# Kernel optimization log

Hardware: AMD Instinct MI355X
Metric: run time of the kernel (lower is better)

The kernel has to match this reference:

```python
import jax, jax.numpy as jnp
import numpy as np

B, I, H = 512, 256, 512
UNFOLDS = 6


def setup_inputs() -> dict:
    key = jax.random.key(0)
    ks = jax.random.split(key, 13)
    u = lambda k, shape, lo, hi: jax.random.uniform(k, shape, jnp.float32, lo, hi)
    sensory_erev = (2.0 * jax.random.randint(ks[3], (I, H), 0, 2) - 1.0).astype(jnp.float32)
    erev = (2.0 * jax.random.randint(ks[7], (H, H), 0, 2) - 1.0).astype(jnp.float32)
    return {
        "inputs": jax.random.normal(ks[0], (B, I), jnp.float32),
        "state": jax.random.normal(ks[1], (B, H), jnp.float32),
        "sensory_mu": u(ks[2], (I, H), 0.3, 0.8),
        "sensory_sigma": u(ks[4], (I, H), 3.0, 8.0),
        "sensory_W": u(ks[5], (I, H), 0.01, 1.0),
        "sensory_erev": sensory_erev,
        "mu": u(ks[6], (H, H), 0.3, 0.8),
        "sigma": u(ks[8], (H, H), 3.0, 8.0),
        "W": u(ks[9], (H, H), 0.01, 1.0),
        "erev": erev,
        "vleak": u(ks[10], (H,), -0.2, 0.2),
        "gleak": jnp.ones((H,), jnp.float32),
        "cm": jnp.full((H,), 0.5, jnp.float32),
    }


def reference(inputs, state, sensory_mu, sensory_sigma, sensory_W, sensory_erev,
              mu, sigma, W, erev, vleak, gleak, cm):
    # Sensory synapse currents (computed once): (B, I, H) broadcast
    sensory_act = jax.nn.sigmoid((inputs[:, :, None] - sensory_mu[None]) * sensory_sigma[None])
    sensory_w_act = sensory_W[None] * sensory_act                      # (B, I, H)
    w_num_sensory = jnp.sum(sensory_w_act * sensory_erev[None], axis=1)  # (B, H)
    w_den_sensory = jnp.sum(sensory_w_act, axis=1)                        # (B, H)

    def step(v_pre, _):
        # recurrent synapse gating: (B, H_pre, H_post)
        act = jax.nn.sigmoid((v_pre[:, :, None] - mu[None]) * sigma[None])
        w_act = W[None] * act
        w_num = jnp.sum(w_act * erev[None], axis=1) + w_num_sensory
        w_den = jnp.sum(w_act, axis=1) + w_den_sensory
        numerator = cm * v_pre + gleak * vleak + w_num
        denominator = cm + gleak + w_den
        return numerator / (denominator + 1e-8), None

    v_pre, _ = jax.lax.scan(step, state, None, length=UNFOLDS)
    return v_pre
```

## Files before the change

kernel.cpp:

```cpp
#include <hip/hip_runtime.h>

#define LTC_B 512
#define LTC_H 512
#define LTC_I 256

static constexpr float kL2E = 1.4426950408889634f;

struct alignas(16) HPair { _Float16 a0, a1, c0, c1, wz0, wz1, wd0, wd1; };

typedef unsigned int u32;
#define AS_G __attribute__((address_space(1)))
#define AS_L __attribute__((address_space(3)))

__device__ __forceinline__ void ldg_lds16(const void* g, void* l) {
    __builtin_amdgcn_global_load_lds((const AS_G u32*)g, (AS_L u32*)l, 16, 0, 0);
}

template<int K>
__global__ void ltc_prep(const float* __restrict__ mu, const float* __restrict__ sigma,
                         const float* __restrict__ W, const float* __restrict__ erev,
                         HPair* __restrict__ slab) {
    const int t = blockIdx.x * 256 + threadIdx.x;
    if (t >= K * 256) return;
    const int hh   = t & 63;
    const int rest = t >> 6;
    const int jp   = rest & (K / 2 - 1);
    const int ht   = rest / (K / 2);
    const int h    = ht * 64 + hh;
    const int g0   = (2 * jp) * LTC_H + h;
    const int g1   = g0 + LTC_H;
    HPair o;
    o.a0 = (_Float16)(-sigma[g0] * kL2E);
    o.a1 = (_Float16)(-sigma[g1] * kL2E);
    o.c0 = (_Float16)(mu[g0] * sigma[g0] * kL2E);
    o.c1 = (_Float16)(mu[g1] * sigma[g1] * kL2E);
    o.wz0 = (_Float16)(W[g0] * erev[g0]);
    o.wz1 = (_Float16)(W[g1] * erev[g1]);
    o.wd0 = (_Float16)(W[g0]);
    o.wd1 = (_Float16)(W[g1]);
    slab[t] = o;
}

template<int K, bool RECUR>
__global__ __launch_bounds__(256, 4)
void ltc_pass(const float* __restrict__ vsrc,
              const HPair* __restrict__ slab,
              const float* __restrict__ snum, const float* __restrict__ sden,
              const float* __restrict__ vleak, const float* __restrict__ gleak,
              const float* __restrict__ cm,
              float* __restrict__ onum, float* __restrict__ oden,
              float* __restrict__ vout)
{
    __shared__ HPair wbuf[2][16 * 64];
    const int tid  = threadIdx.x;
    const int lane = tid & 63;
    const int wu   = __builtin_amdgcn_readfirstlane(tid >> 6);
    const int ht   = blockIdx.x;
    const int b    = blockIdx.y * 4 + wu;
    const float* __restrict__ vrow = vsrc + (size_t)b * K;

    constexpr int NC = K / 32;
    const int rot = (int)((blockIdx.x + 7u * blockIdx.y) & (NC - 1));
    const char* slabt = (const char*)slab + (size_t)ht * (K * 512);

    {
        const char* src = slabt + rot * 16384 + wu * 4096;
        char* dst = (char*)&wbuf[0][0] + wu * 4096;
        #pragma unroll
        for (int rr = 0; rr < 4; ++rr)
            ldg_lds16(src + rr * 1024 + lane * 16, dst + rr * 1024);
    }

    float na = 0.f, da = 0.f;

    #pragma unroll
    for (int i = 0; i < NC; ++i) {
        const int c = (rot + i) & (NC - 1);
        __syncthreads();
        if (i + 1 < NC) {
            const int cn = (rot + i + 1) & (NC - 1);
            const char* src = slabt + cn * 16384 + wu * 4096;
            char* dst = (char*)&wbuf[(i + 1) & 1][0] + wu * 4096;
            #pragma unroll
            for (int rr = 0; rr < 4; ++rr)
                ldg_lds16(src + rr * 1024 + lane * 16, dst + rr * 1024);
        }
        const HPair* wb = &wbuf[i & 1][0];
        const float* __restrict__ vch = vrow + c * 32;

        HPair pr[16];
        #pragma unroll
        for (int jj = 0; jj < 16; ++jj) pr[jj] = wb[jj * 64 + lane];

        #pragma unroll
        for (int jj = 0; jj < 16; ++jj) {
            const float vj0 = vch[2 * jj];
            const float vj1 = vch[2 * jj + 1];
            const float t0 = fmaf((float)pr[jj].a0, vj0, (float)pr[jj].c0);
            const float t1 = fmaf((float)pr[jj].a1, vj1, (float)pr[jj].c1);
            const float e0 = __builtin_amdgcn_exp2f(t0);
            const float e1 = __builtin_amdgcn_exp2f(t1);
            const float d0 = 1.0f + e0;
            const float d1 = 1.0f + e1;
            const float rr = __builtin_amdgcn_rcpf(d0 * d1);
            const float s0 = rr * d1;
            const float s1 = rr * d0;
            na = fmaf((float)pr[jj].wz0, s0, na);
            da = fmaf((float)pr[jj].wd0, s0, da);
            na = fmaf((float)pr[jj].wz1, s1, na);
            da = fmaf((float)pr[jj].wd1, s1, da);
        }
    }

    const int h  = ht * 64 + lane;
    const int bh = b * LTC_H + h;
    if constexpr (RECUR) {
        const float gl = gleak[h], vl = vleak[h], c0 = cm[h];
        const float vp = vsrc[bh];
        const float num = fmaf(c0, vp, gl * vl) + na + snum[bh];
        const float den = c0 + gl + da + sden[bh];
        vout[bh] = num * __builtin_amdgcn_rcpf(den + 1e-8f);
    } else {
        onum[bh] = na;
        oden[bh] = da;
    }
}

extern "C" void kernel_launch(void* const* d_in, const int* in_sizes, int n_in,
                              void* d_out, int out_size, void* d_ws, size_t ws_size,
                              hipStream_t stream) {
    const float* inputs = (const float*)d_in[0];
    const float* state  = (const float*)d_in[1];
    const float* smu    = (const float*)d_in[2];
    const float* ssig   = (const float*)d_in[3];
    const float* sW     = (const float*)d_in[4];
    const float* serev  = (const float*)d_in[5];
    const float* mu     = (const float*)d_in[6];
    const float* sig    = (const float*)d_in[7];
    const float* W      = (const float*)d_in[8];
    const float* erev   = (const float*)d_in[9];
    const float* vleak  = (const float*)d_in[10];
    const float* gleak  = (const float*)d_in[11];
    const float* cm     = (const float*)d_in[12];

    float* out  = (float*)d_out;
    char*  ws   = (char*)d_ws;
    float* snum = (float*)(ws);
    float* sden = (float*)(ws + 1 * 1048576);
    float* vA   = (float*)(ws + 2 * 1048576);
    HPair* rslab = (HPair*)(ws + 3 * 1048576);
    HPair* sslab = (HPair*)(ws + 5 * 1048576);

    ltc_prep<LTC_H><<<LTC_H * 256 / 256, 256, 0, stream>>>(mu, sig, W, erev, rslab);
    ltc_prep<LTC_I><<<LTC_I * 256 / 256, 256, 0, stream>>>(smu, ssig, sW, serev, sslab);

    dim3 grid(LTC_H / 64, LTC_B / 4);
    dim3 blk(256);

    ltc_pass<LTC_I, false><<<grid, blk, 0, stream>>>(
        inputs, sslab, nullptr, nullptr, nullptr, nullptr, nullptr,
        snum, sden, nullptr);

    const float* vin = state;
    float* targets[6] = {vA, out, vA, out, vA, out};
    for (int s = 0; s < 6; ++s) {
        ltc_pass<LTC_H, true><<<grid, blk, 0, stream>>>(
            vin, rslab, snum, sden, vleak, gleak, cm,
            nullptr, nullptr, targets[s]);
        vin = targets[s];
    }
}
```

Before: 333.3 us.

## Split K reduction across two wave groups per block with LDS combine

```diff
diff --git a/kernel.cpp b/kernel.cpp
--- a/kernel.cpp
+++ b/kernel.cpp
@@ -42,7 +42,7 @@
 }
 
 template<int K, bool RECUR>
-__global__ __launch_bounds__(256, 4)
+__global__ __launch_bounds__(512, 8)
 void ltc_pass(const float* __restrict__ vsrc,
               const HPair* __restrict__ slab,
               const float* __restrict__ snum, const float* __restrict__ sden,
@@ -51,49 +51,51 @@
               float* __restrict__ onum, float* __restrict__ oden,
               float* __restrict__ vout)
 {
-    __shared__ HPair wbuf[2][16 * 64];
+    __shared__ HPair wbuf[2][2][8 * 64];
+    __shared__ float comb[4][2][64];
+
     const int tid  = threadIdx.x;
     const int lane = tid & 63;
     const int wu   = __builtin_amdgcn_readfirstlane(tid >> 6);
+    const int bw   = wu & 3;
+    const int jh   = wu >> 2;
     const int ht   = blockIdx.x;
-    const int b    = blockIdx.y * 4 + wu;
-    const float* __restrict__ vrow = vsrc + (size_t)b * K;
+    const int b    = blockIdx.y * 4 + bw;
+    const float* __restrict__ vrow = vsrc + (size_t)b * K + jh * (K / 2);
 
-    constexpr int NC = K / 32;
-    const int rot = (int)((blockIdx.x + 7u * blockIdx.y) & (NC - 1));
-    const char* slabt = (const char*)slab + (size_t)ht * (K * 512);
+    constexpr int NCH = K / 32;
+    const int rot = (int)((blockIdx.x + 7u * blockIdx.y) & (NCH - 1));
+    const char* slabt = (const char*)slab + (size_t)ht * (K * 512) + (size_t)jh * (K * 256);
 
     {
-        const char* src = slabt + rot * 16384 + wu * 4096;
-        char* dst = (char*)&wbuf[0][0] + wu * 4096;
-        #pragma unroll
-        for (int rr = 0; rr < 4; ++rr)
-            ldg_lds16(src + rr * 1024 + lane * 16, dst + rr * 1024);
+        const char* src = slabt + rot * 8192 + bw * 2048;
+        char* dst = (char*)&wbuf[jh][0][0] + bw * 2048;
+        ldg_lds16(src + lane * 16, dst);
+        ldg_lds16(src + 1024 + lane * 16, dst + 1024);
     }
 
     float na = 0.f, da = 0.f;
 
     #pragma unroll
-    for (int i = 0; i < NC; ++i) {
-        const int c = (rot + i) & (NC - 1);
+    for (int i = 0; i < NCH; ++i) {
+        const int c = (rot + i) & (NCH - 1);
         __syncthreads();
-        if (i + 1 < NC) {
-            const int cn = (rot + i + 1) & (NC - 1);
-            const char* src = slabt + cn * 16384 + wu * 4096;
-            char* dst = (char*)&wbuf[(i + 1) & 1][0] + wu * 4096;
-            #pragma unroll
-            for (int rr = 0; rr < 4; ++rr)
-                ldg_lds16(src + rr * 1024 + lane * 16, dst + rr * 1024);
+        if (i + 1 < NCH) {
+            const int cn = (rot + i + 1) & (NCH - 1);
+            const char* src = slabt + cn * 8192 + bw * 2048;
+            char* dst = (char*)&wbuf[jh][(i + 1) & 1][0] + bw * 2048;
+            ldg_lds16(src + lane * 16, dst);
+            ldg_lds16(src + 1024 + lane * 16, dst + 1024);
         }
-        const HPair* wb = &wbuf[i & 1][0];
-        const float* __restrict__ vch = vrow + c * 32;
+        const HPair* wb = &wbuf[jh][i & 1][0];
+        const float* __restrict__ vch = vrow + c * 16;
 
-        HPair pr[16];
+        HPair pr[8];
         #pragma unroll
-        for (int jj = 0; jj < 16; ++jj) pr[jj] = wb[jj * 64 + lane];
+        for (int jj = 0; jj < 8; ++jj) pr[jj] = wb[jj * 64 + lane];
 
         #pragma unroll
-        for (int jj = 0; jj < 16; ++jj) {
+        for (int jj = 0; jj < 8; ++jj) {
             const float vj0 = vch[2 * jj];
             const float vj1 = vch[2 * jj + 1];
             const float t0 = fmaf((float)pr[jj].a0, vj0, (float)pr[jj].c0);
@@ -112,17 +114,23 @@
         }
     }
 
-    const int h  = ht * 64 + lane;
-    const int bh = b * LTC_H + h;
-    if constexpr (RECUR) {
-        const float gl = gleak[h], vl = vleak[h], c0 = cm[h];
-        const float vp = vsrc[bh];
-        const float num = fmaf(c0, vp, gl * vl) + na + snum[bh];
-        const float den = c0 + gl + da + sden[bh];
-        vout[bh] = num * __builtin_amdgcn_rcpf(den + 1e-8f);
-    } else {
-        onum[bh] = na;
-        oden[bh] = da;
+    if (jh == 1) { comb[bw][0][lane] = na; comb[bw][1][lane] = da; }
+    __syncthreads();
+    if (jh == 0) {
+        na += comb[bw][0][lane];
+        da += comb[bw][1][lane];
+        const int h  = ht * 64 + lane;
+        const int bh = b * LTC_H + h;
+        if constexpr (RECUR) {
+            const float gl = gleak[h], vl = vleak[h], c0 = cm[h];
+            const float vp = vsrc[bh];
+            const float num = fmaf(c0, vp, gl * vl) + na + snum[bh];
+            const float den = c0 + gl + da + sden[bh];
+            vout[bh] = num * __builtin_amdgcn_rcpf(den + 1e-8f);
+        } else {
+            onum[bh] = na;
+            oden[bh] = da;
+        }
     }
 }
 
@@ -155,7 +163,7 @@
     ltc_prep<LTC_I><<<LTC_I * 256 / 256, 256, 0, stream>>>(smu, ssig, sW, serev, sslab);
 
     dim3 grid(LTC_H / 64, LTC_B / 4);
-    dim3 blk(256);
+    dim3 blk(512);
 
     ltc_pass<LTC_I, false><<<grid, blk, 0, stream>>>(
         inputs, sslab, nullptr, nullptr, nullptr, nullptr, nullptr,
```

Result: no change. 327.1 us (-1.9%).

## Split K across 8 waves, reuse each weight load for 4 batch rows

Applied to the files above, without the earlier changes.

```diff
diff --git a/kernel.cpp b/kernel.cpp
--- a/kernel.cpp
+++ b/kernel.cpp
@@ -7,14 +7,6 @@
 static constexpr float kL2E = 1.4426950408889634f;
 
 struct alignas(16) HPair { _Float16 a0, a1, c0, c1, wz0, wz1, wd0, wd1; };
-
-typedef unsigned int u32;
-#define AS_G __attribute__((address_space(1)))
-#define AS_L __attribute__((address_space(3)))
-
-__device__ __forceinline__ void ldg_lds16(const void* g, void* l) {
-    __builtin_amdgcn_global_load_lds((const AS_G u32*)g, (AS_L u32*)l, 16, 0, 0);
-}
 
 template<int K>
 __global__ void ltc_prep(const float* __restrict__ mu, const float* __restrict__ sigma,
@@ -42,7 +34,7 @@
 }
 
 template<int K, bool RECUR>
-__global__ __launch_bounds__(256, 4)
+__global__ __launch_bounds__(512, 8)
 void ltc_pass(const float* __restrict__ vsrc,
               const HPair* __restrict__ slab,
               const float* __restrict__ snum, const float* __restrict__ sden,
@@ -51,78 +43,105 @@
               float* __restrict__ onum, float* __restrict__ oden,
               float* __restrict__ vout)
 {
-    __shared__ HPair wbuf[2][16 * 64];
+    constexpr int JQ = 8;
+    constexpr int PW = (K / 2) / JQ;
+    constexpr int CP = 2;
+    constexpr int NC = PW / CP;
+
+    __shared__ float comb[JQ][4][64][2];
+
     const int tid  = threadIdx.x;
     const int lane = tid & 63;
     const int wu   = __builtin_amdgcn_readfirstlane(tid >> 6);
     const int ht   = blockIdx.x;
-    const int b    = blockIdx.y * 4 + wu;
-    const float* __restrict__ vrow = vsrc + (size_t)b * K;
+    const int b0   = blockIdx.y * 4;
 
-    constexpr int NC = K / 32;
-    const int rot = (int)((blockIdx.x + 7u * blockIdx.y) & (NC - 1));
-    const char* slabt = (const char*)slab + (size_t)ht * (K * 512);
+    const HPair* __restrict__ wp =
+        slab + ((size_t)ht * (K / 2) + (size_t)wu * PW) * 64 + lane;
+    const float* __restrict__ v0 = vsrc + (size_t)(b0 + 0) * K + wu * (2 * PW);
+    const float* __restrict__ v1 = vsrc + (size_t)(b0 + 1) * K + wu * (2 * PW);
+    const float* __restrict__ v2 = vsrc + (size_t)(b0 + 2) * K + wu * (2 * PW);
+    const float* __restrict__ v3 = vsrc + (size_t)(b0 + 3) * K + wu * (2 * PW);
 
-    {
-        const char* src = slabt + rot * 16384 + wu * 4096;
-        char* dst = (char*)&wbuf[0][0] + wu * 4096;
-        #pragma unroll
-        for (int rr = 0; rr < 4; ++rr)
-            ldg_lds16(src + rr * 1024 + lane * 16, dst + rr * 1024);
-    }
+    float na0 = 0.f, da0 = 0.f, na1 = 0.f, da1 = 0.f;
+    float na2 = 0.f, da2 = 0.f, na3 = 0.f, da3 = 0.f;
 
-    float na = 0.f, da = 0.f;
+    auto evalp = [&](const HPair& pr, int p) {
+        const float a0f = (float)pr.a0, a1f = (float)pr.a1;
+        const float c0f = (float)pr.c0, c1f = (float)pr.c1;
+        const float wz0f = (float)pr.wz0, wz1f = (float)pr.wz1;
+        const float wd0f = (float)pr.wd0, wd1f = (float)pr.wd1;
+#define LTC_ONEB(vb, nab, dab)                                             \
+        {                                                                  \
+            const float t0 = fmaf(a0f, vb[2 * p], c0f);                    \
+            const float t1 = fmaf(a1f, vb[2 * p + 1], c1f);                \
+            const float e0 = __builtin_amdgcn_exp2f(t0);                   \
+            const float e1 = __builtin_amdgcn_exp2f(t1);                   \
+            const float d0 = 1.0f + e0;                                    \
+            const float d1 = 1.0f + e1;                                    \
+            const float rr = __builtin_amdgcn_rcpf(d0 * d1);               \
+            const float s0 = rr * d1;                                      \
+            const float s1 = rr * d0;                                      \
+            nab = fmaf(wz0f, s0, nab);                                     \
+            dab = fmaf(wd0f, s0, dab);                                     \
+            nab = fmaf(wz1f, s1, nab);                                     \
+            dab = fmaf(wd1f, s1, dab);                                     \
+        }
+        LTC_ONEB(v0, na0, da0)
+        LTC_ONEB(v1, na1, da1)
+        LTC_ONEB(v2, na2, da2)
+        LTC_ONEB(v3, na3, da3)
+#undef LTC_ONEB
+    };
+
+    HPair bA[CP], bB[CP];
+    #pragma unroll
+    for (int q = 0; q < CP; ++q) bA[q] = wp[(0 * CP + q) * 64];
+    #pragma unroll
+    for (int q = 0; q < CP; ++q) bB[q] = wp[(1 * CP + q) * 64];
 
     #pragma unroll
-    for (int i = 0; i < NC; ++i) {
-        const int c = (rot + i) & (NC - 1);
-        __syncthreads();
-        if (i + 1 < NC) {
-            const int cn = (rot + i + 1) & (NC - 1);
-            const char* src = slabt + cn * 16384 + wu * 4096;
-            char* dst = (char*)&wbuf[(i + 1) & 1][0] + wu * 4096;
+    for (int ch = 0; ch < NC; ch += 2) {
+        #pragma unroll
+        for (int q = 0; q < CP; ++q) evalp(bA[q], ch * CP + q);
+        if (ch + 2 < NC) {
             #pragma unroll
-            for (int rr = 0; rr < 4; ++rr)
-                ldg_lds16(src + rr * 1024 + lane * 16, dst + rr * 1024);
+            for (int q = 0; q < CP; ++q) bA[q] = wp[((ch + 2) * CP + q) * 64];
         }
-        const HPair* wb = &wbuf[i & 1][0];
-        const float* __restrict__ vch = vrow + c * 32;
-
-        HPair pr[16];
         #pragma unroll
-        for (int jj = 0; jj < 16; ++jj) pr[jj] = wb[jj * 64 + lane];
-
-        #pragma unroll
-        for (int jj = 0; jj < 16; ++jj) {
-            const float vj0 = vch[2 * jj];
-            const float vj1 = vch[2 * jj + 1];
-            const float t0 = fmaf((float)pr[jj].a0, vj0, (float)pr[jj].c0);
-            const float t1 = fmaf((float)pr[jj].a1, vj1, (float)pr[jj].c1);
-            const float e0 = __builtin_amdgcn_exp2f(t0);
-            const float e1 = __builtin_amdgcn_exp2f(t1);
-            const float d0 = 1.0f + e0;
-            const float d1 = 1.0f + e1;
-            const float rr = __builtin_amdgcn_rcpf(d0 * d1);
-            const float s0 = rr * d1;
-            const float s1 = rr * d0;
-            na = fmaf((float)pr[jj].wz0, s0, na);
-            da = fmaf((float)pr[jj].wd0, s0, da);
-            na = fmaf((float)pr[jj].wz1, s1, na);
-            da = fmaf((float)pr[jj].wd1, s1, da);
+        for (int q = 0; q < CP; ++q) evalp(bB[q], (ch + 1) * CP + q);
+        if (ch + 3 < NC) {
+            #pragma unroll
+            for (int q = 0; q < CP; ++q) bB[q] = wp[((ch + 3) * CP + q) * 64];
         }
     }
 
-    const int h  = ht * 64 + lane;
-    const int bh = b * LTC_H + h;
-    if constexpr (RECUR) {
-        const float gl = gleak[h], vl = vleak[h], c0 = cm[h];
-        const float vp = vsrc[bh];
-        const float num = fmaf(c0, vp, gl * vl) + na + snum[bh];
-        const float den = c0 + gl + da + sden[bh];
-        vout[bh] = num * __builtin_amdgcn_rcpf(den + 1e-8f);
-    } else {
-        onum[bh] = na;
-        oden[bh] = da;
+    comb[wu][0][lane][0] = na0; comb[wu][0][lane][1] = da0;
+    comb[wu][1][lane][0] = na1; comb[wu][1][lane][1] = da1;
+    comb[wu][2][lane][0] = na2; comb[wu][2][lane][1] = da2;
+    comb[wu][3][lane][0] = na3; comb[wu][3][lane][1] = da3;
+    __syncthreads();
+
+    if (wu < 4) {
+        float na = 0.f, da = 0.f;
+        #pragma unroll
+        for (int jq = 0; jq < JQ; ++jq) {
+            na += comb[jq][wu][lane][0];
+            da += comb[jq][wu][lane][1];
+        }
+        const int b  = b0 + wu;
+        const int h  = ht * 64 + lane;
+        const int bh = b * LTC_H + h;
+        if constexpr (RECUR) {
+            const float gl = gleak[h], vl = vleak[h], c0 = cm[h];
+            const float vp = vsrc[bh];
+            const float num = fmaf(c0, vp, gl * vl) + na + snum[bh];
+            const float den = c0 + gl + da + sden[bh];
+            vout[bh] = num * __builtin_amdgcn_rcpf(den + 1e-8f);
+        } else {
+            onum[bh] = na;
+            oden[bh] = da;
+        }
     }
 }
 
@@ -155,7 +174,7 @@
     ltc_prep<LTC_I><<<LTC_I * 256 / 256, 256, 0, stream>>>(smu, ssig, sW, serev, sslab);
 
     dim3 grid(LTC_H / 64, LTC_B / 4);
-    dim3 blk(256);
+    dim3 blk(512);
 
     ltc_pass<LTC_I, false><<<grid, blk, 0, stream>>>(
         inputs, sslab, nullptr, nullptr, nullptr, nullptr, nullptr,
```

New measurement: 305.8 us. 8.3% less time.
